# Performance work log

Measured on AMD Instinct MI355X. Metric: run time of the kernel, lower is better.

Reference implementation:

```python
import jax, jax.numpy as jnp
import numpy as np
import math

NUM_HEADS = 8
HEAD_DIM = 32  # num_units 256 / 8 heads
TIME_DIM = 8
NEG_BIG = -2.0 ** 32 + 1.0


def _ffn(x, W1, b1, W2, b2):
    # two-layer relu MLP: 1 -> time_dim -> time_dim
    h = jax.nn.relu(x @ W1 + b1)
    return jax.nn.relu(h @ W2 + b2)


def _time_gsm_kernel(t, pW1, pb1, pW2, pb2, sW1, sb1, sW2, sb2, bW1, bb1, bW2, bb2):
    # t: [B, L] timestamps -> kernel [B, L, L]
    tt = t[..., None]  # [B, L, 1]
    period = _ffn(tt, pW1, pb1, pW2, pb2)        # [B, L, td]
    qpq = (2.0 * math.pi) * period * tt           # [B, L, td]
    period_diff = qpq[:, :, None, :] - qpq[:, None, :, :]  # [B, Lq, Lk, td]
    cos_enc = jnp.cos(period_diff)
    sigma = _ffn(tt, sW1, sb1, sW2, sb2)          # [B, L, td]
    sq = sigma[:, :, None, :] + 1e-6              # [B, Lq, 1, td] bcast
    sk = sigma[:, None, :, :] + 1e-6              # [B, 1, Lk, td] bcast
    denom = sq ** 2 + sk ** 2
    t_diff = t[:, :, None] - t[:, None, :]        # [B, Lq, Lk]
    exp_enc = jnp.exp(-(t_diff[..., None] ** 2) / denom)
    local_enc = jnp.sqrt(2.0 * sq * sk / denom)
    basis = _ffn(tt, bW1, bb1, bW2, bb2)          # [B, L, td]
    basis_qk = basis[:, :, None, :] * basis[:, None, :, :]
    return jnp.sum(basis_qk * local_enc * exp_enc * cos_enc, axis=-1)  # [B, L, L]


def setup_inputs() -> dict:
    key = jax.random.key(0)
    ks = jax.random.split(key, 20)
    B, L, U = 4, 1024, 256
    td = TIME_DIM
    inp = {
        'query_input': jax.random.normal(ks[0], (B, L, U), dtype=jnp.float32),
        'input_tensor': jax.random.normal(ks[1], (B, L, U), dtype=jnp.float32),
        'input_mask': jnp.ones((B, L), dtype=jnp.int32),
        'time_inputs': jax.random.uniform(ks[2], (B, L), dtype=jnp.float32) * 100.0,
        'att_bias': jnp.zeros((1,), dtype=jnp.int32),
        'Wq': jax.random.normal(ks[3], (U, U), dtype=jnp.float32) * 0.05,
        'Wk': jax.random.normal(ks[4], (U, U), dtype=jnp.float32) * 0.05,
        'Wv': jax.random.normal(ks[5], (U, U), dtype=jnp.float32) * 0.05,
    }
    names = ['p', 's', 'b']
    i = 6
    for n in names:
        inp[n + 'W1'] = jax.random.normal(ks[i], (1, td), dtype=jnp.float32) * 0.5; i += 1
        inp[n + 'b1'] = jnp.zeros((td,), dtype=jnp.float32)
        inp[n + 'W2'] = jax.random.normal(ks[i], (td, td), dtype=jnp.float32) * 0.5; i += 1
        inp[n + 'b2'] = jnp.zeros((td,), dtype=jnp.float32)
    return inp


def reference(query_input, input_tensor, input_mask, time_inputs, att_bias,
              Wq, Wk, Wv,
              pW1, pb1, pW2, pb2, sW1, sb1, sW2, sb2, bW1, bb1, bW2, bb2):
    B, Lq, U = query_input.shape
    Lk = input_tensor.shape[1]
    H, dh = NUM_HEADS, HEAD_DIM

    Q = (query_input @ Wq).reshape(B, Lq, H, dh).transpose(0, 2, 1, 3)  # [B,H,Lq,dh]
    K = (input_tensor @ Wk).reshape(B, Lk, H, dh).transpose(0, 2, 1, 3)
    V = (input_tensor @ Wv).reshape(B, Lk, H, dh).transpose(0, 2, 1, 3)

    scale = 1.0 / math.sqrt(dh)
    scores = jnp.einsum('bhqd,bhkd->bhqk', Q, K) * scale  # [B,H,Lq,Lk]

    tk = _time_gsm_kernel(time_inputs, pW1, pb1, pW2, pb2,
                          sW1, sb1, sW2, sb2, bW1, bb1, bW2, bb2)  # [B,Lq,Lk]
    scores = scores + tk[:, None, :, :] * scale

    # key padding mask: zero-norm keys get -inf-like score
    key_masks = jnp.sign(jnp.sum(jnp.abs(K), axis=-1))  # [B,H,Lk]
    scores = jnp.where(key_masks[:, :, None, :] == 0.0, NEG_BIG, scores)

    # direction == 'forward': allow strictly row > col (strict causal)
    idx = jnp.arange(Lk)
    causal = (idx[:, None] > idx[None, :]).astype(scores.dtype)  # [Lq,Lk]
    scores = scores + (1.0 - causal) * -10000.0

    attn = jax.nn.softmax(scores, axis=-1)

    query_masks = jnp.sign(jnp.sum(jnp.abs(Q), axis=-1))  # [B,H,Lq]
    attn = attn * query_masks[..., None]
    # dropout rate 0.0 -> identity

    out = jnp.einsum('bhqk,bhkd->bhqd', attn, V)
    out = out.transpose(0, 2, 1, 3).reshape(B, Lq, U)
    out = out * input_mask.astype(jnp.float32)[..., None]
    return out
```

## Files before the change

kernel.cpp:

```cpp
#include <hip/hip_runtime.h>
#include <math.h>

#define B_DIM 4
#define L_DIM 1024
#define H_DIM 8
#define D_DIM 32
#define TD 8
#define NTILES_TOT 1056
#define SCALE 0.17677669529663687f
#define TWO_PI_F 6.2831853071795864769f

typedef unsigned short ushort_t;
typedef __attribute__((ext_vector_type(8))) short short8v;
typedef __attribute__((ext_vector_type(4))) float f32x4;

__device__ __forceinline__ int ntiles_of(int qt) { return (qt >> 1) + 1; }
__device__ __forceinline__ int off_of(int qt) {
  int m = qt >> 1;
  return (qt & 1) ? (m + 1) * (m + 1) : m * m + m;
}

__device__ __forceinline__ ushort_t f2bf(float f) {
  unsigned u = __builtin_bit_cast(unsigned, f);
  u += 0x7FFFu + ((u >> 16) & 1u);
  return (ushort_t)(u >> 16);
}
__device__ __forceinline__ float bf2f(ushort_t h) {
  return __builtin_bit_cast(float, ((unsigned)h) << 16);
}
__device__ __forceinline__ short8v pack84(float4 a, float4 b) {
  short8v r;
  r[0] = (short)f2bf(a.x); r[1] = (short)f2bf(a.y);
  r[2] = (short)f2bf(a.z); r[3] = (short)f2bf(a.w);
  r[4] = (short)f2bf(b.x); r[5] = (short)f2bf(b.y);
  r[6] = (short)f2bf(b.z); r[7] = (short)f2bf(b.w);
  return r;
}

__global__ __launch_bounds__(256) void prep_kernel(
    const float* __restrict__ t_in,
    const float* __restrict__ pW1, const float* __restrict__ pb1,
    const float* __restrict__ pW2, const float* __restrict__ pb2,
    const float* __restrict__ sW1, const float* __restrict__ sb1,
    const float* __restrict__ sW2, const float* __restrict__ sb2,
    const float* __restrict__ bW1, const float* __restrict__ bb1,
    const float* __restrict__ bW2, const float* __restrict__ bb2,
    float* __restrict__ ptf, float* __restrict__ sg, float* __restrict__ bs,
    const float* __restrict__ Xq, const float* __restrict__ Xi,
    ushort_t* __restrict__ Xfq, ushort_t* __restrict__ Xfi,
    const float* __restrict__ Wq, const float* __restrict__ Wk,
    const float* __restrict__ Wv, ushort_t* __restrict__ Wf) {
  const int blk = blockIdx.x;
  const int tid = threadIdx.x;
  if (blk < 512) {
    const int lin = blk * 256 + tid;
    const int i = lin >> 5;
    const int slot = lin & 31;
    const int z = slot >> 3, e = slot & 7;
    if (z == 3) return;
    const float* W1 = (z == 0) ? pW1 : (z == 1) ? sW1 : bW1;
    const float* b1 = (z == 0) ? pb1 : (z == 1) ? sb1 : bb1;
    const float* W2 = (z == 0) ? pW2 : (z == 1) ? sW2 : bW2;
    const float* b2 = (z == 0) ? pb2 : (z == 1) ? sb2 : bb2;
    const double t = (double)t_in[i];
    double acc = (double)b2[e];
#pragma unroll
    for (int d = 0; d < 8; ++d) {
      double hv = t * (double)W1[d] + (double)b1[d];
      hv = hv > 0.0 ? hv : 0.0;
      acc += hv * (double)W2[d * 8 + e];
    }
    acc = acc > 0.0 ? acc : 0.0;
    const size_t o = (size_t)i * TD + e;
    if (z == 0) {
      double pt = acc * t;
      ptf[o] = (float)(pt - floor(pt));
    } else if (z == 1) {
      sg[o] = (float)(acc + 1e-6);
    } else {
      bs[o] = (float)acc;
    }
  } else if (blk < 1536) {
    const int xb = blk - 512;
    const float* X = (xb < 512) ? Xq : Xi;
    ushort_t* O = (xb < 512) ? Xfq : Xfi;
    const int lin = (xb & 511) * 256 + tid;
    const int row = lin >> 5, q = lin & 31;
    const float* src = &X[(size_t)row * 256 + q * 8];
    short8v f = pack84(*(const float4*)src, *(const float4*)(src + 4));
    size_t idx = ((size_t)((row >> 4) * 8 + (q >> 2)) * 64 + (q & 3) * 16 + (row & 15)) * 8;
    *(short8v*)&O[idx] = f;
  } else {
    const int wb = blk - 1536;
    const int z = wb >> 5;
    const float* W = (z == 0) ? Wq : (z == 1) ? Wk : Wv;
    const int lin = (wb & 31) * 256 + tid;
    const int kt = lin >> 10, g = (lin >> 8) & 3, n = lin & 255;
    short8v f;
#pragma unroll
    for (int i2 = 0; i2 < 8; ++i2)
      f[i2] = (short)f2bf(W[(size_t)(kt * 32 + g * 8 + i2) * 256 + n]);
    size_t idx = ((size_t)((z * 8 + kt) * 16 + (n >> 4)) * 64 + g * 16 + (n & 15)) * 8;
    *(short8v*)&Wf[idx] = f;
  }
}

__global__ __launch_bounds__(256) void work_kernel(
    const ushort_t* __restrict__ Xfq, const ushort_t* __restrict__ Xfi,
    const ushort_t* __restrict__ Wf,
    ushort_t* __restrict__ Qf, ushort_t* __restrict__ Kf,
    ushort_t* __restrict__ Vf,
    const float* __restrict__ ptf, const float* __restrict__ sg,
    const float* __restrict__ bs, const float* __restrict__ t_in,
    float* __restrict__ tkbuf) {
  __shared__ float ptq[16][TD], ptk[32][9];
  __shared__ float qs[16][TD], qb[16][TD];
  __shared__ float ks[32][9], kb[32][9];
  __shared__ float trow[16], tcol[32];
  const int blk = blockIdx.x;
  const int tid = threadIdx.x;

  if (blk < 384) {
    const int z = blk >> 7;
    const int rem = blk & 127;
    const int m0t = (rem & 31) * 8;
    const int n0 = (rem >> 5) * 64;
    const ushort_t* Xf = (z == 0) ? Xfq : Xfi;
    const int w = tid >> 6, l = tid & 63, lg = l >> 4, lc = l & 15;
    const int wm = w >> 1, wn = w & 1;

    f32x4 acc[4][2];
#pragma unroll
    for (int mi = 0; mi < 4; ++mi)
#pragma unroll
      for (int ni = 0; ni < 2; ++ni) acc[mi][ni] = (f32x4){0.f, 0.f, 0.f, 0.f};

    for (int kt0 = 0; kt0 < 8; ++kt0) {
      short8v a[4], bfr[2];
#pragma unroll
      for (int mi = 0; mi < 4; ++mi)
        a[mi] = *(const short8v*)&Xf[((size_t)(m0t + wm * 4 + mi) * 8 + kt0) * 512 + l * 8];
#pragma unroll
      for (int ni = 0; ni < 2; ++ni)
        bfr[ni] = *(const short8v*)&Wf[((size_t)(z * 8 + kt0) * 16 + (n0 >> 4) + wn * 2 + ni) * 512 + l * 8];
#pragma unroll
      for (int mi = 0; mi < 4; ++mi)
#pragma unroll
        for (int ni = 0; ni < 2; ++ni)
          acc[mi][ni] = __builtin_amdgcn_mfma_f32_16x16x32_bf16(a[mi], bfr[ni], acc[mi][ni], 0, 0, 0);
    }

#pragma unroll
    for (int mi = 0; mi < 4; ++mi) {
#pragma unroll
      for (int ni = 0; ni < 2; ++ni) {
        const int col = n0 + wn * 32 + ni * 16 + lc;
        const int hh = col >> 5, d = col & 31;
#pragma unroll
        for (int r = 0; r < 4; ++r) {
          const int row = (m0t + wm * 4 + mi) * 16 + lg * 4 + r;
          const int bb = row >> 10, lr = row & (L_DIM - 1);
          const ushort_t bv = f2bf(acc[mi][ni][r]);
          if (z == 2) {
            Vf[(((size_t)(bb * H_DIM + hh) * 32 + (lr >> 5)) * 2 + (d >> 4)) * 512 +
               (((lr >> 3) & 3) * 16 + (d & 15)) * 8 + (lr & 7)] = bv;
          } else {
            ushort_t* of16 = (z == 0) ? Qf : Kf;
            of16[((size_t)((bb * H_DIM + hh) * 64 + (lr >> 4))) * 512 +
                 ((d >> 3) * 16 + (lr & 15)) * 8 + (d & 7)] = bv;
          }
        }
      }
    }
  } else {
    const int lin = blk - 384;
    const int b = lin / NTILES_TOT;
    const int t1 = lin - b * NTILES_TOT;
    int m = (int)sqrtf((float)t1 + 1.0f);
    while (m * m + m > t1) --m;
    while ((m + 1) * (m + 1) + (m + 1) <= t1) ++m;
    const int rem = t1 - (m * m + m);
    int qt, kt;
    if (rem <= m) { qt = 2 * m; kt = rem; }
    else          { qt = 2 * m + 1; kt = rem - (m + 1); }

    const int q0 = qt << 4, k0 = kt << 5;
    if (tid < 16 * TD) {
      int i = tid >> 3, d = tid & 7;
      size_t base = (size_t)(b * L_DIM + q0 + i) * TD + d;
      ptq[i][d] = ptf[base]; qs[i][d] = sg[base]; qb[i][d] = bs[base];
    }
    {
      int j = tid >> 3, d = tid & 7;
      size_t base = (size_t)(b * L_DIM + k0 + j) * TD + d;
      ptk[j][d] = ptf[base]; ks[j][d] = sg[base]; kb[j][d] = bs[base];
    }
    if (tid < 16) trow[tid] = t_in[b * L_DIM + q0 + tid];
    if (tid < 32) tcol[tid] = t_in[b * L_DIM + k0 + tid];
    __syncthreads();
    float* dst = &tkbuf[(size_t)(b * NTILES_TOT + off_of(qt) + kt) * 512];
#pragma unroll
    for (int pp = 0; pp < 2; ++pp) {
      int idx = tid + (pp << 8);
      int lr2 = (idx >> 2) & 63;
      int r = idx & 3;
      int i = ((lr2 >> 4) << 2) | r;
      int j = ((idx >> 8) << 4) | (lr2 & 15);
      float td2 = trow[i] - tcol[j];
      td2 *= td2;
      float a = 0.f;
#pragma unroll
      for (int d = 0; d < TD; ++d) {
        float sqd = qs[i][d], skd = ks[j][d];
        float denom = sqd * sqd + skd * skd;
        float inv = __builtin_amdgcn_rcpf(denom);
        float ee = __expf(-td2 * inv);
        float le = __builtin_amdgcn_sqrtf(2.f * sqd * skd * inv);
        float dq = ptq[i][d] - ptk[j][d];
        float ce = __cosf(TWO_PI_F * dq);
        a += qb[i][d] * kb[j][d] * (le * ee * ce);
      }
      dst[idx] = a;
    }
  }
}

__global__ __launch_bounds__(256) void attn_row0_kernel(
    const ushort_t* __restrict__ Qf, const ushort_t* __restrict__ Kf,
    const ushort_t* __restrict__ Vf, const float* __restrict__ tkbuf,
    const int* __restrict__ imask, float* __restrict__ out) {
  __shared__ __align__(16) ushort_t lds_p[4][1024];
  __shared__ float p_s[L_DIM];
  __shared__ float qsh[D_DIM];
  __shared__ float red[8][33];
  __shared__ float rtmp[4];

  const int h = blockIdx.y;
  const int b = blockIdx.z;
  const int tid = threadIdx.x;
  const int fb = (b * H_DIM + h) * 64;
  const int vb = (b * H_DIM + h) * 32;

  if (blockIdx.x == 16) {
    if (tid < D_DIM)
      qsh[tid] = bf2f(Qf[(size_t)fb * 512 + (tid >> 3) * 128 + (tid & 7)]);
    __syncthreads();

    float lmax = -1e30f;
    for (int j = tid; j < L_DIM; j += 256) {
      int i = j & 15;
      float tkv = tkbuf[(size_t)(b * NTILES_TOT + off_of(j >> 4)) * 512 +
                        (((i >> 2) << 6) | (i & 3))];
      const ushort_t* kp = &Kf[(size_t)(fb + (j >> 4)) * 512 + (j & 15) * 8];
      float dot = 0.f;
#pragma unroll
      for (int o = 0; o < 4; ++o) {
        short8v kv = *(const short8v*)&kp[o * 128];
#pragma unroll
        for (int u = 0; u < 8; ++u) dot += qsh[o * 8 + u] * bf2f((ushort_t)kv[u]);
      }
      float sc = (dot + tkv) * SCALE;
      p_s[j] = sc;
      lmax = fmaxf(lmax, sc);
    }
#pragma unroll
    for (int o = 1; o < 64; o <<= 1) lmax = fmaxf(lmax, __shfl_xor(lmax, o));
    if ((tid & 63) == 0) rtmp[tid >> 6] = lmax;
    __syncthreads();
    const float bmax = fmaxf(fmaxf(rtmp[0], rtmp[1]), fmaxf(rtmp[2], rtmp[3]));
    __syncthreads();

    float lsumv = 0.f;
    for (int j = tid; j < L_DIM; j += 256) {
      float pv = __expf(p_s[j] - bmax);
      p_s[j] = pv;
      lsumv += pv;
    }
#pragma unroll
    for (int o = 1; o < 64; o <<= 1) lsumv += __shfl_xor(lsumv, o);
    if ((tid & 63) == 0) rtmp[tid >> 6] = lsumv;
    __syncthreads();
    const float bsum = rtmp[0] + rtmp[1] + rtmp[2] + rtmp[3];

    const int g = tid >> 5, d = tid & 31;
    float a = 0.f;
    for (int j = g * 128; j < g * 128 + 128; ++j) {
      float v = bf2f(Vf[(((size_t)(vb + (j >> 5))) * 2 + (d >> 4)) * 512 +
                        (((j >> 3) & 3) * 16 + (d & 15)) * 8 + (j & 7)]);
      a = fmaf(p_s[j], v, a);
    }
    red[g][d] = a;
    __syncthreads();
    if (tid < D_DIM) {
      float acc = 0.f;
#pragma unroll
      for (int gg = 0; gg < 8; ++gg) acc += red[gg][tid];
      float qabs = 0.f;
#pragma unroll
      for (int dd = 0; dd < D_DIM; ++dd) qabs += fabsf(qsh[dd]);
      const float qmv = qabs > 0.f ? 1.f : 0.f;
      out[((size_t)b * L_DIM) * 256 + h * D_DIM + tid] =
          acc * (1.0f / bsum) * qmv * (float)imask[b * L_DIM];
    }
    return;
  }

  const int qc = (b >= 2) ? (int)blockIdx.x : 15 - (int)blockIdx.x;
  const int w = tid >> 6;
  const int l = tid & 63;
  const int lg = l >> 4;
  const int lc = l & 15;
  const int qbase = qc * 64 + w * 16;
  const int qt = qbase >> 4;

  short8v qfrag = *(const short8v*)&Qf[((size_t)(fb + qt)) * 512 + l * 8];
  float qabs_l = 0.f;
#pragma unroll
  for (int j = 0; j < 8; ++j) qabs_l += fabsf(bf2f((ushort_t)qfrag[j]));
  qabs_l += __shfl_xor(qabs_l, 16);
  qabs_l += __shfl_xor(qabs_l, 32);
  const float qm = (qabs_l > 0.f) ? 1.f : 0.f;

  f32x4 O0 = {0.f, 0.f, 0.f, 0.f};
  f32x4 O1 = {0.f, 0.f, 0.f, 0.f};
  float mrow[4] = {-1e30f, -1e30f, -1e30f, -1e30f};
  float lrow[4] = {0.f, 0.f, 0.f, 0.f};
  const float* tk_qt = &tkbuf[(size_t)(b * NTILES_TOT + off_of(qt)) * 512];
  ushort_t* Pw = lds_p[w];

  for (int kc = 0; kc <= qc; ++kc) {
    float s[4][4];
    const bool diag = (kc == qc);
#pragma unroll
    for (int kt = 0; kt < 4; ++kt) {
      short8v kfrag = *(const short8v*)&Kf[((size_t)(fb + kc * 4 + kt)) * 512 + l * 8];
      f32x4 z4 = {0.f, 0.f, 0.f, 0.f};
      f32x4 sv = __builtin_amdgcn_mfma_f32_16x16x32_bf16(qfrag, kfrag, z4, 0, 0, 0);
      float4 tk4 = *(const float4*)&tk_qt[(size_t)(kc * 2 + (kt >> 1)) * 512 + (kt & 1) * 256 + l * 4];
      float tka[4] = {tk4.x, tk4.y, tk4.z, tk4.w};
      const int col = kc * 64 + kt * 16 + lc;
#pragma unroll
      for (int r = 0; r < 4; ++r) {
        float val = (sv[r] + tka[r]) * SCALE;
        if (diag && col >= qbase + lg * 4 + r) val = -10000.0f;
        s[kt][r] = val;
      }
    }

#pragma unroll
    for (int r = 0; r < 4; ++r) {
      float tmax = fmaxf(fmaxf(s[0][r], s[1][r]), fmaxf(s[2][r], s[3][r]));
      tmax = fmaxf(tmax, __shfl_xor(tmax, 1));
      tmax = fmaxf(tmax, __shfl_xor(tmax, 2));
      tmax = fmaxf(tmax, __shfl_xor(tmax, 4));
      tmax = fmaxf(tmax, __shfl_xor(tmax, 8));
      float mnew = fmaxf(mrow[r], tmax);
      float cf = __expf(mrow[r] - mnew);
      mrow[r] = mnew;
      float p0 = __expf(s[0][r] - mnew);
      float p1 = __expf(s[1][r] - mnew);
      float p2 = __expf(s[2][r] - mnew);
      float p3 = __expf(s[3][r] - mnew);
      float psum = (p0 + p1) + (p2 + p3);
      psum += __shfl_xor(psum, 1);
      psum += __shfl_xor(psum, 2);
      psum += __shfl_xor(psum, 4);
      psum += __shfl_xor(psum, 8);
      lrow[r] = lrow[r] * cf + psum;
      O0[r] *= cf;
      O1[r] *= cf;
      const int pb = ((lc >> 3) << 7) + ((lg * 4 + r) << 3) + (lc & 7);
      Pw[pb] = f2bf(p0);
      Pw[pb + 256] = f2bf(p1);
      Pw[pb + 512] = f2bf(p2);
      Pw[pb + 768] = f2bf(p3);
    }

#pragma unroll
    for (int kh = 0; kh < 2; ++kh) {
      short8v pfrag = *(const short8v*)&Pw[(kh * 64 + l) * 8];
      const size_t vbase = ((size_t)(vb + kc * 2 + kh)) * 1024 + l * 8;
      short8v vf0 = *(const short8v*)&Vf[vbase];
      short8v vf1 = *(const short8v*)&Vf[vbase + 512];
      O0 = __builtin_amdgcn_mfma_f32_16x16x32_bf16(pfrag, vf0, O0, 0, 0, 0);
      O1 = __builtin_amdgcn_mfma_f32_16x16x32_bf16(pfrag, vf1, O1, 0, 0, 0);
    }
  }

#pragma unroll
  for (int r = 0; r < 4; ++r) {
    const int rr = lg * 4 + r;
    const int qrow = qbase + rr;
    float qmr = __shfl(qm, rr);
    float im = (float)imask[b * L_DIM + qrow];
    float scl = (1.f / lrow[r]) * qmr * im;
    if (qrow != 0) {
      float* op = &out[((size_t)(b * L_DIM + qrow)) * 256 + h * D_DIM];
      op[lc] = O0[r] * scl;
      op[16 + lc] = O1[r] * scl;
    }
  }
}

extern "C" void kernel_launch(void* const* d_in, const int* in_sizes, int n_in,
                              void* d_out, int out_size, void* d_ws, size_t ws_size,
                              hipStream_t stream) {
  (void)in_sizes; (void)n_in; (void)out_size; (void)ws_size;
  const float* query = (const float*)d_in[0];
  const float* input = (const float*)d_in[1];
  const int* imask = (const int*)d_in[2];
  const float* t_in = (const float*)d_in[3];
  const float* Wq = (const float*)d_in[5];
  const float* Wk = (const float*)d_in[6];
  const float* Wv = (const float*)d_in[7];
  const float* pW1 = (const float*)d_in[8],  *pb1 = (const float*)d_in[9];
  const float* pW2 = (const float*)d_in[10], *pb2 = (const float*)d_in[11];
  const float* sW1 = (const float*)d_in[12], *sb1 = (const float*)d_in[13];
  const float* sW2 = (const float*)d_in[14], *sb2 = (const float*)d_in[15];
  const float* bW1 = (const float*)d_in[16], *bb1 = (const float*)d_in[17];
  const float* bW2 = (const float*)d_in[18], *bb2 = (const float*)d_in[19];
  float* out = (float*)d_out;

  const int M = B_DIM * L_DIM;
  char* p = (char*)d_ws;
  ushort_t* Qf = (ushort_t*)p;  p += (size_t)M * 256 * 2;
  ushort_t* Kf = (ushort_t*)p;  p += (size_t)M * 256 * 2;
  ushort_t* Vf = (ushort_t*)p;  p += (size_t)M * 256 * 2;
  ushort_t* Xfq = (ushort_t*)p; p += (size_t)M * 256 * 2;
  ushort_t* Xfi = (ushort_t*)p; p += (size_t)M * 256 * 2;
  ushort_t* Wfb = (ushort_t*)p; p += (size_t)3 * 256 * 256 * 2;
  float* ptf = (float*)p;       p += (size_t)M * TD * 4;
  float* sg = (float*)p;        p += (size_t)M * TD * 4;
  float* bs = (float*)p;        p += (size_t)M * TD * 4;
  float* tkbuf = (float*)p;

  prep_kernel<<<1632, 256, 0, stream>>>(
      t_in, pW1, pb1, pW2, pb2, sW1, sb1, sW2, sb2, bW1, bb1, bW2, bb2,
      ptf, sg, bs, query, input, Xfq, Xfi, Wq, Wk, Wv, Wfb);
  work_kernel<<<384 + B_DIM * NTILES_TOT, 256, 0, stream>>>(
      Xfq, Xfi, Wfb, Qf, Kf, Vf, ptf, sg, bs, t_in, tkbuf);
  attn_row0_kernel<<<dim3(17, H_DIM, B_DIM), 256, 0, stream>>>(
      Qf, Kf, Vf, tkbuf, imask, out);
}
```

Baseline: 62.08 us.

## Fuse prep into work kernel, fold scale upstream, prefetch attention fragments

Removes the separate prep kernel. The projection GEMM now reads fp32 X directly and converts it to bf16 in registers, while W tiles are staged through double-buffered LDS. The three time-MLP outputs are recomputed per tile into shared memory instead of being read from global buffers. The attention scale is folded into Q and the time kernel, and the attention loop double-buffers its K, time and V fragments in registers with s_setprio around the MFMAs. This cuts one launch and the intermediate global traffic, at the cost of redundant double-precision MLP work per tile and higher register pressure.

```diff
diff --git a/kernel.cpp b/kernel.cpp
--- a/kernel.cpp
+++ b/kernel.cpp
@@ -8,7 +8,6 @@
 #define TD 8
 #define NTILES_TOT 1056
 #define SCALE 0.17677669529663687f
-#define TWO_PI_F 6.2831853071795864769f
 
 typedef unsigned short ushort_t;
 typedef __attribute__((ext_vector_type(8))) short short8v;
@@ -37,117 +36,75 @@
   return r;
 }
 
-__global__ __launch_bounds__(256) void prep_kernel(
-    const float* __restrict__ t_in,
+__global__ __launch_bounds__(256) void work_kernel(
+    const float* __restrict__ Xq, const float* __restrict__ Xi,
+    const float* __restrict__ Wq, const float* __restrict__ Wk,
+    const float* __restrict__ Wv, const float* __restrict__ t_in,
     const float* __restrict__ pW1, const float* __restrict__ pb1,
     const float* __restrict__ pW2, const float* __restrict__ pb2,
     const float* __restrict__ sW1, const float* __restrict__ sb1,
     const float* __restrict__ sW2, const float* __restrict__ sb2,
     const float* __restrict__ bW1, const float* __restrict__ bb1,
     const float* __restrict__ bW2, const float* __restrict__ bb2,
-    float* __restrict__ ptf, float* __restrict__ sg, float* __restrict__ bs,
-    const float* __restrict__ Xq, const float* __restrict__ Xi,
-    ushort_t* __restrict__ Xfq, ushort_t* __restrict__ Xfi,
-    const float* __restrict__ Wq, const float* __restrict__ Wk,
-    const float* __restrict__ Wv, ushort_t* __restrict__ Wf) {
-  const int blk = blockIdx.x;
-  const int tid = threadIdx.x;
-  if (blk < 512) {
-    const int lin = blk * 256 + tid;
-    const int i = lin >> 5;
-    const int slot = lin & 31;
-    const int z = slot >> 3, e = slot & 7;
-    if (z == 3) return;
-    const float* W1 = (z == 0) ? pW1 : (z == 1) ? sW1 : bW1;
-    const float* b1 = (z == 0) ? pb1 : (z == 1) ? sb1 : bb1;
-    const float* W2 = (z == 0) ? pW2 : (z == 1) ? sW2 : bW2;
-    const float* b2 = (z == 0) ? pb2 : (z == 1) ? sb2 : bb2;
-    const double t = (double)t_in[i];
-    double acc = (double)b2[e];
-#pragma unroll
-    for (int d = 0; d < 8; ++d) {
-      double hv = t * (double)W1[d] + (double)b1[d];
-      hv = hv > 0.0 ? hv : 0.0;
-      acc += hv * (double)W2[d * 8 + e];
-    }
-    acc = acc > 0.0 ? acc : 0.0;
-    const size_t o = (size_t)i * TD + e;
-    if (z == 0) {
-      double pt = acc * t;
-      ptf[o] = (float)(pt - floor(pt));
-    } else if (z == 1) {
-      sg[o] = (float)(acc + 1e-6);
-    } else {
-      bs[o] = (float)acc;
-    }
-  } else if (blk < 1536) {
-    const int xb = blk - 512;
-    const float* X = (xb < 512) ? Xq : Xi;
-    ushort_t* O = (xb < 512) ? Xfq : Xfi;
-    const int lin = (xb & 511) * 256 + tid;
-    const int row = lin >> 5, q = lin & 31;
-    const float* src = &X[(size_t)row * 256 + q * 8];
-    short8v f = pack84(*(const float4*)src, *(const float4*)(src + 4));
-    size_t idx = ((size_t)((row >> 4) * 8 + (q >> 2)) * 64 + (q & 3) * 16 + (row & 15)) * 8;
-    *(short8v*)&O[idx] = f;
-  } else {
-    const int wb = blk - 1536;
-    const int z = wb >> 5;
-    const float* W = (z == 0) ? Wq : (z == 1) ? Wk : Wv;
-    const int lin = (wb & 31) * 256 + tid;
-    const int kt = lin >> 10, g = (lin >> 8) & 3, n = lin & 255;
-    short8v f;
-#pragma unroll
-    for (int i2 = 0; i2 < 8; ++i2)
-      f[i2] = (short)f2bf(W[(size_t)(kt * 32 + g * 8 + i2) * 256 + n]);
-    size_t idx = ((size_t)((z * 8 + kt) * 16 + (n >> 4)) * 64 + g * 16 + (n & 15)) * 8;
-    *(short8v*)&Wf[idx] = f;
-  }
-}
-
-__global__ __launch_bounds__(256) void work_kernel(
-    const ushort_t* __restrict__ Xfq, const ushort_t* __restrict__ Xfi,
-    const ushort_t* __restrict__ Wf,
     ushort_t* __restrict__ Qf, ushort_t* __restrict__ Kf,
-    ushort_t* __restrict__ Vf,
-    const float* __restrict__ ptf, const float* __restrict__ sg,
-    const float* __restrict__ bs, const float* __restrict__ t_in,
-    float* __restrict__ tkbuf) {
-  __shared__ float ptq[16][TD], ptk[32][9];
-  __shared__ float qs[16][TD], qb[16][TD];
-  __shared__ float ks[32][9], kb[32][9];
-  __shared__ float trow[16], tcol[32];
+    ushort_t* __restrict__ Vf, float* __restrict__ tkbuf) {
+  __shared__ __align__(16) char smem[8192];
   const int blk = blockIdx.x;
   const int tid = threadIdx.x;
 
   if (blk < 384) {
     const int z = blk >> 7;
     const int rem = blk & 127;
-    const int m0t = (rem & 31) * 8;
+    const int m0 = (rem & 31) * 128;
     const int n0 = (rem >> 5) * 64;
-    const ushort_t* Xf = (z == 0) ? Xfq : Xfi;
+    const float* X = (z == 0) ? Xq : Xi;
+    const float* W = (z == 0) ? Wq : (z == 1) ? Wk : Wv;
+    ushort_t* wl = (ushort_t*)smem;
     const int w = tid >> 6, l = tid & 63, lg = l >> 4, lc = l & 15;
     const int wm = w >> 1, wn = w & 1;
 
+    auto stageW = [&](int kt, int buf) {
+      ushort_t* wb = wl + buf * 2048;
+#pragma unroll
+      for (int half = 0; half < 2; ++half) {
+        int f = half * 256 + tid;
+        int k = f >> 4;
+        int nc = (f & 15) << 2;
+        float4 v4 = *(const float4*)&W[(size_t)(kt * 32 + k) * 256 + n0 + nc];
+        float va[4] = {v4.x, v4.y, v4.z, v4.w};
+#pragma unroll
+        for (int u = 0; u < 4; ++u) {
+          int n6 = nc + u;
+          wb[(((n6 >> 4) * 4 + (k >> 3)) * 16 + (n6 & 15)) * 8 + (k & 7)] = f2bf(va[u]);
+        }
+      }
+    };
+
     f32x4 acc[4][2];
 #pragma unroll
     for (int mi = 0; mi < 4; ++mi)
 #pragma unroll
       for (int ni = 0; ni < 2; ++ni) acc[mi][ni] = (f32x4){0.f, 0.f, 0.f, 0.f};
 
+    stageW(0, 0);
+    __syncthreads();
     for (int kt0 = 0; kt0 < 8; ++kt0) {
+      if (kt0 < 7) stageW(kt0 + 1, (kt0 + 1) & 1);
       short8v a[4], bfr[2];
 #pragma unroll
-      for (int mi = 0; mi < 4; ++mi)
-        a[mi] = *(const short8v*)&Xf[((size_t)(m0t + wm * 4 + mi) * 8 + kt0) * 512 + l * 8];
+      for (int mi = 0; mi < 4; ++mi) {
+        const float* xp = &X[(size_t)(m0 + (wm * 4 + mi) * 16 + lc) * 256 + kt0 * 32 + lg * 8];
+        a[mi] = pack84(*(const float4*)xp, *(const float4*)(xp + 4));
+      }
 #pragma unroll
       for (int ni = 0; ni < 2; ++ni)
-        bfr[ni] = *(const short8v*)&Wf[((size_t)(z * 8 + kt0) * 16 + (n0 >> 4) + wn * 2 + ni) * 512 + l * 8];
+        bfr[ni] = *(const short8v*)&wl[(kt0 & 1) * 2048 + ((wn * 2 + ni) * 64 + l) * 8];
 #pragma unroll
       for (int mi = 0; mi < 4; ++mi)
 #pragma unroll
         for (int ni = 0; ni < 2; ++ni)
           acc[mi][ni] = __builtin_amdgcn_mfma_f32_16x16x32_bf16(a[mi], bfr[ni], acc[mi][ni], 0, 0, 0);
+      __syncthreads();
     }
 
 #pragma unroll
@@ -158,9 +115,11 @@
         const int hh = col >> 5, d = col & 31;
 #pragma unroll
         for (int r = 0; r < 4; ++r) {
-          const int row = (m0t + wm * 4 + mi) * 16 + lg * 4 + r;
+          const int row = m0 + (wm * 4 + mi) * 16 + lg * 4 + r;
           const int bb = row >> 10, lr = row & (L_DIM - 1);
-          const ushort_t bv = f2bf(acc[mi][ni][r]);
+          float v = acc[mi][ni][r];
+          if (z == 0) v *= SCALE;
+          const ushort_t bv = f2bf(v);
           if (z == 2) {
             Vf[(((size_t)(bb * H_DIM + hh) * 32 + (lr >> 5)) * 2 + (d >> 4)) * 512 +
                (((lr >> 3) & 3) * 16 + (d & 15)) * 8 + (lr & 7)] = bv;
@@ -183,21 +142,46 @@
     int qt, kt;
     if (rem <= m) { qt = 2 * m; kt = rem; }
     else          { qt = 2 * m + 1; kt = rem - (m + 1); }
-
     const int q0 = qt << 4, k0 = kt << 5;
-    if (tid < 16 * TD) {
-      int i = tid >> 3, d = tid & 7;
-      size_t base = (size_t)(b * L_DIM + q0 + i) * TD + d;
-      ptq[i][d] = ptf[base]; qs[i][d] = sg[base]; qb[i][d] = bs[base];
-    }
-    {
-      int j = tid >> 3, d = tid & 7;
-      size_t base = (size_t)(b * L_DIM + k0 + j) * TD + d;
-      ptk[j][d] = ptf[base]; ks[j][d] = sg[base]; kb[j][d] = bs[base];
-    }
+
+    float* ptq = (float*)(smem);
+    float* qs  = (float*)(smem + 512);
+    float* qb  = (float*)(smem + 1024);
+    float* ptk = (float*)(smem + 1536);
+    float* ks  = (float*)(smem + 2688);
+    float* kb  = (float*)(smem + 3840);
+    float* trow= (float*)(smem + 4992);
+    float* tcol= (float*)(smem + 5056);
+
     if (tid < 16) trow[tid] = t_in[b * L_DIM + q0 + tid];
     if (tid < 32) tcol[tid] = t_in[b * L_DIM + k0 + tid];
-    __syncthreads();
+    for (int s = tid; s < 1152; s += 256) {
+      const int z = s / 384;
+      const int rm = s - z * 384;
+      const int p = rm >> 3, e = rm & 7;
+      const int gi = (p < 16) ? (q0 + p) : (k0 + p - 16);
+      const double t = (double)t_in[b * L_DIM + gi];
+      const float* W1 = (z == 0) ? pW1 : (z == 1) ? sW1 : bW1;
+      const float* b1 = (z == 0) ? pb1 : (z == 1) ? sb1 : bb1;
+      const float* W2 = (z == 0) ? pW2 : (z == 1) ? sW2 : bW2;
+      const float* b2 = (z == 0) ? pb2 : (z == 1) ? sb2 : bb2;
+      double acc = (double)b2[e];
+#pragma unroll
+      for (int d = 0; d < 8; ++d) {
+        double hv = t * (double)W1[d] + (double)b1[d];
+        hv = hv > 0.0 ? hv : 0.0;
+        acc += hv * (double)W2[d * 8 + e];
+      }
+      acc = acc > 0.0 ? acc : 0.0;
+      float val;
+      if (z == 0) { double pt = acc * t; val = (float)(pt - floor(pt)); }
+      else if (z == 1) val = (float)(acc + 1e-6);
+      else val = (float)acc;
+      if (p < 16) (z == 0 ? ptq : z == 1 ? qs : qb)[p * 8 + e] = val;
+      else        (z == 0 ? ptk : z == 1 ? ks : kb)[(p - 16) * 9 + e] = val;
+    }
+    __syncthreads();
+
     float* dst = &tkbuf[(size_t)(b * NTILES_TOT + off_of(qt) + kt) * 512];
 #pragma unroll
     for (int pp = 0; pp < 2; ++pp) {
@@ -211,19 +195,25 @@
       float a = 0.f;
 #pragma unroll
       for (int d = 0; d < TD; ++d) {
-        float sqd = qs[i][d], skd = ks[j][d];
+        float sqd = qs[i * 8 + d], skd = ks[j * 9 + d];
         float denom = sqd * sqd + skd * skd;
         float inv = __builtin_amdgcn_rcpf(denom);
         float ee = __expf(-td2 * inv);
         float le = __builtin_amdgcn_sqrtf(2.f * sqd * skd * inv);
-        float dq = ptq[i][d] - ptk[j][d];
-        float ce = __cosf(TWO_PI_F * dq);
-        a += qb[i][d] * kb[j][d] * (le * ee * ce);
-      }
-      dst[idx] = a;
+        float dq = ptq[i * 8 + d] - ptk[j * 9 + d];
+        float ce = __builtin_amdgcn_cosf(dq);
+        a += qb[i * 8 + d] * kb[j * 9 + d] * (le * ee * ce);
+      }
+      dst[idx] = a * SCALE;
     }
   }
 }
+
+struct AFrags {
+  short8v k0, k1, k2, k3;
+  float4 t0, t1, t2, t3;
+  short8v v0, v1, v2, v3;
+};
 
 __global__ __launch_bounds__(256) void attn_row0_kernel(
     const ushort_t* __restrict__ Qf, const ushort_t* __restrict__ Kf,
@@ -259,7 +249,7 @@
 #pragma unroll
         for (int u = 0; u < 8; ++u) dot += qsh[o * 8 + u] * bf2f((ushort_t)kv[u]);
       }
-      float sc = (dot + tkv) * SCALE;
+      float sc = dot + tkv;
       p_s[j] = sc;
       lmax = fmaxf(lmax, sc);
     }
@@ -328,25 +318,46 @@
   const float* tk_qt = &tkbuf[(size_t)(b * NTILES_TOT + off_of(qt)) * 512];
   ushort_t* Pw = lds_p[w];
 
-  for (int kc = 0; kc <= qc; ++kc) {
+  auto loadf = [&](AFrags& F, int kc) {
+    const size_t kb_ = ((size_t)(fb + kc * 4)) * 512 + l * 8;
+    F.k0 = *(const short8v*)&Kf[kb_];
+    F.k1 = *(const short8v*)&Kf[kb_ + 512];
+    F.k2 = *(const short8v*)&Kf[kb_ + 1024];
+    F.k3 = *(const short8v*)&Kf[kb_ + 1536];
+    const size_t tb_ = (size_t)(kc * 2) * 512 + l * 4;
+    F.t0 = *(const float4*)&tk_qt[tb_];
+    F.t1 = *(const float4*)&tk_qt[tb_ + 256];
+    F.t2 = *(const float4*)&tk_qt[tb_ + 512];
+    F.t3 = *(const float4*)&tk_qt[tb_ + 768];
+    const size_t vb_ = ((size_t)(vb + kc * 2)) * 1024 + l * 8;
+    F.v0 = *(const short8v*)&Vf[vb_];
+    F.v1 = *(const short8v*)&Vf[vb_ + 512];
+    F.v2 = *(const short8v*)&Vf[vb_ + 1024];
+    F.v3 = *(const short8v*)&Vf[vb_ + 1536];
+  };
+
+  auto iterate = [&](const AFrags& F, int kc, bool diag) {
+    f32x4 z4 = {0.f, 0.f, 0.f, 0.f};
+    __builtin_amdgcn_s_setprio(1);
+    f32x4 sv0 = __builtin_amdgcn_mfma_f32_16x16x32_bf16(qfrag, F.k0, z4, 0, 0, 0);
+    f32x4 sv1 = __builtin_amdgcn_mfma_f32_16x16x32_bf16(qfrag, F.k1, z4, 0, 0, 0);
+    f32x4 sv2 = __builtin_amdgcn_mfma_f32_16x16x32_bf16(qfrag, F.k2, z4, 0, 0, 0);
+    f32x4 sv3 = __builtin_amdgcn_mfma_f32_16x16x32_bf16(qfrag, F.k3, z4, 0, 0, 0);
+    __builtin_amdgcn_s_setprio(0);
     float s[4][4];
-    const bool diag = (kc == qc);
+    const float* tka[4] = {(const float*)&F.t0, (const float*)&F.t1,
+                           (const float*)&F.t2, (const float*)&F.t3};
+    const f32x4* svs[4] = {&sv0, &sv1, &sv2, &sv3};
 #pragma unroll
     for (int kt = 0; kt < 4; ++kt) {
-      short8v kfrag = *(const short8v*)&Kf[((size_t)(fb + kc * 4 + kt)) * 512 + l * 8];
-      f32x4 z4 = {0.f, 0.f, 0.f, 0.f};
-      f32x4 sv = __builtin_amdgcn_mfma_f32_16x16x32_bf16(qfrag, kfrag, z4, 0, 0, 0);
-      float4 tk4 = *(const float4*)&tk_qt[(size_t)(kc * 2 + (kt >> 1)) * 512 + (kt & 1) * 256 + l * 4];
-      float tka[4] = {tk4.x, tk4.y, tk4.z, tk4.w};
       const int col = kc * 64 + kt * 16 + lc;
 #pragma unroll
       for (int r = 0; r < 4; ++r) {
-        float val = (sv[r] + tka[r]) * SCALE;
+        float val = (*svs[kt])[r] + tka[kt][r];
         if (diag && col >= qbase + lg * 4 + r) val = -10000.0f;
         s[kt][r] = val;
       }
     }
-
 #pragma unroll
     for (int r = 0; r < 4; ++r) {
       float tmax = fmaxf(fmaxf(s[0][r], s[1][r]), fmaxf(s[2][r], s[3][r]));
@@ -375,16 +386,27 @@
       Pw[pb + 512] = f2bf(p2);
       Pw[pb + 768] = f2bf(p3);
     }
-
-#pragma unroll
-    for (int kh = 0; kh < 2; ++kh) {
-      short8v pfrag = *(const short8v*)&Pw[(kh * 64 + l) * 8];
-      const size_t vbase = ((size_t)(vb + kc * 2 + kh)) * 1024 + l * 8;
-      short8v vf0 = *(const short8v*)&Vf[vbase];
-      short8v vf1 = *(const short8v*)&Vf[vbase + 512];
-      O0 = __builtin_amdgcn_mfma_f32_16x16x32_bf16(pfrag, vf0, O0, 0, 0, 0);
-      O1 = __builtin_amdgcn_mfma_f32_16x16x32_bf16(pfrag, vf1, O1, 0, 0, 0);
-    }
+    short8v pf0 = *(const short8v*)&Pw[l * 8];
+    short8v pf1 = *(const short8v*)&Pw[(64 + l) * 8];
+    __builtin_amdgcn_s_setprio(1);
+    O0 = __builtin_amdgcn_mfma_f32_16x16x32_bf16(pf0, F.v0, O0, 0, 0, 0);
+    O1 = __builtin_amdgcn_mfma_f32_16x16x32_bf16(pf0, F.v1, O1, 0, 0, 0);
+    O0 = __builtin_amdgcn_mfma_f32_16x16x32_bf16(pf1, F.v2, O0, 0, 0, 0);
+    O1 = __builtin_amdgcn_mfma_f32_16x16x32_bf16(pf1, F.v3, O1, 0, 0, 0);
+    __builtin_amdgcn_s_setprio(0);
+  };
+
+  AFrags fA, fB;
+  loadf(fA, 0);
+  int kc = 0;
+  while (true) {
+    if (kc + 1 <= qc) loadf(fB, kc + 1);
+    iterate(fA, kc, kc == qc);
+    if (kc + 1 > qc) break;
+    if (kc + 2 <= qc) loadf(fA, kc + 2);
+    iterate(fB, kc + 1, kc + 1 == qc);
+    if (kc + 2 > qc) break;
+    kc += 2;
   }
 
 #pragma unroll
@@ -426,19 +448,12 @@
   ushort_t* Qf = (ushort_t*)p;  p += (size_t)M * 256 * 2;
   ushort_t* Kf = (ushort_t*)p;  p += (size_t)M * 256 * 2;
   ushort_t* Vf = (ushort_t*)p;  p += (size_t)M * 256 * 2;
-  ushort_t* Xfq = (ushort_t*)p; p += (size_t)M * 256 * 2;
-  ushort_t* Xfi = (ushort_t*)p; p += (size_t)M * 256 * 2;
-  ushort_t* Wfb = (ushort_t*)p; p += (size_t)3 * 256 * 256 * 2;
-  float* ptf = (float*)p;       p += (size_t)M * TD * 4;
-  float* sg = (float*)p;        p += (size_t)M * TD * 4;
-  float* bs = (float*)p;        p += (size_t)M * TD * 4;
   float* tkbuf = (float*)p;
 
-  prep_kernel<<<1632, 256, 0, stream>>>(
-      t_in, pW1, pb1, pW2, pb2, sW1, sb1, sW2, sb2, bW1, bb1, bW2, bb2,
-      ptf, sg, bs, query, input, Xfq, Xfi, Wq, Wk, Wv, Wfb);
   work_kernel<<<384 + B_DIM * NTILES_TOT, 256, 0, stream>>>(
-      Xfq, Xfi, Wfb, Qf, Kf, Vf, ptf, sg, bs, t_in, tkbuf);
+      query, input, Wq, Wk, Wv, t_in,
+      pW1, pb1, pW2, pb2, sW1, sb1, sW2, sb2, bW1, bb1, bW2, bb2,
+      Qf, Kf, Vf, tkbuf);
   attn_row0_kernel<<<dim3(17, H_DIM, B_DIM), 256, 0, stream>>>(
       Qf, Kf, Vf, tkbuf, imask, out);
 }
```

New measurement: 76.50 us. 1.23x slower.
